# Kernel optimization log

Hardware: AMD Instinct MI355X
Metric: run time of the kernel (lower is better)

The kernel has to match this reference:

```python
import jax, jax.numpy as jnp
import numpy as np

NUM_HEADS = 8
NUM_HYPEREDGES = 64
NODE_DIM = 512
HEAD_DIM = NODE_DIM // NUM_HEADS
SCALING = float(np.sqrt(HEAD_DIM))


def setup_inputs() -> dict:
    key = jax.random.key(0)
    ks = jax.random.split(key, 6)
    B, N, D, M = 16, 4096, NODE_DIM, NUM_HYPEREDGES
    X = jax.random.normal(ks[0], (B, N, D), dtype=jnp.float32)
    # xavier_uniform for prototype_base [M, D]
    lim_p = float(np.sqrt(6.0 / (M + D)))
    prototype_base = jax.random.uniform(ks[1], (M, D), minval=-lim_p, maxval=lim_p, dtype=jnp.float32)
    # context_net: Linear(2D -> M*D), torch default init ~ U(-1/sqrt(fan_in), ...)
    lim_c = 1.0 / float(np.sqrt(2 * D))
    W_ctx = jax.random.uniform(ks[2], (M * D, 2 * D), minval=-lim_c, maxval=lim_c, dtype=jnp.float32)
    b_ctx = jax.random.uniform(ks[3], (M * D,), minval=-lim_c, maxval=lim_c, dtype=jnp.float32)
    # pre_head_proj: Linear(D -> D)
    lim_h = 1.0 / float(np.sqrt(D))
    W_pre = jax.random.uniform(ks[4], (D, D), minval=-lim_h, maxval=lim_h, dtype=jnp.float32)
    b_pre = jax.random.uniform(ks[5], (D,), minval=-lim_h, maxval=lim_h, dtype=jnp.float32)
    return {"X": X, "prototype_base": prototype_base, "W_ctx": W_ctx, "b_ctx": b_ctx,
            "W_pre": W_pre, "b_pre": b_pre}


def reference(X, prototype_base, W_ctx, b_ctx, W_pre, b_pre):
    B, N, D = X.shape
    M, H, hd = NUM_HYPEREDGES, NUM_HEADS, HEAD_DIM
    # context pooling: mean + max over nodes -> [B, 2D]
    ctx = jnp.concatenate([X.mean(axis=1), X.max(axis=1)], axis=-1)
    # per-batch prototype offsets: [B, M, D]
    offsets = (ctx @ W_ctx.T + b_ctx).reshape(B, M, D)
    prototypes = prototype_base[None, :, :] + offsets  # [B, M, D]
    # project nodes
    X_proj = X @ W_pre.T + b_pre  # [B, N, D]
    Xh = X_proj.reshape(B, N, H, hd)       # [B, N, H, hd]
    Ph = prototypes.reshape(B, M, H, hd)   # [B, M, H, hd]
    # per-head attention logits, mean over heads: [B, N, M]
    logits = jnp.einsum('bnhd,bmhd->bnm', Xh, Ph) / (SCALING * H)
    # dropout is identity in eval mode; softmax over the NODE axis (dim=1)
    return jax.nn.softmax(logits, axis=1)
```

## Files before the change

kernel.cpp:

```cpp
#include <hip/hip_runtime.h>
#include <math.h>

#define B_ 16
#define N_ 4096
#define D_ 512
#define M_ 64
#define MD 32768

typedef __attribute__((ext_vector_type(4))) float f32x4;
typedef __attribute__((ext_vector_type(8))) short short8;

#define OFF_PSUM   0
#define OFF_PMAXP  1048576
#define OFF_CTXB   2097152
#define OFF_PB     2105344
#define OFF_WPT    2367488
#define OFF_CB     2498560
#define OFF_GMAX   2499584
#define OFF_GINV   2500608
#define OFF_TPMAX  2501632
#define OFF_TPSUM  2763776
#define OFF_QB     3025920
#define OFF_LGB    3288064

__device__ __forceinline__ unsigned short f2bf(float f) {
    unsigned int u = __float_as_uint(f);
    u += 0x7fffu + ((u >> 16) & 1u);
    return (unsigned short)(u >> 16);
}
__device__ __forceinline__ float bf2f(unsigned short u) {
    return __uint_as_float(((unsigned int)u) << 16);
}

__global__ __launch_bounds__(256) void k_pool(const float* __restrict__ X, float* __restrict__ ws) {
    int b = blockIdx.x >> 6, nc = blockIdx.x & 63, t = threadIdx.x;
    int c = t & 127, p = t >> 7;
    const float4* X4 = (const float4*)X;
    float4 s = make_float4(0.f, 0.f, 0.f, 0.f);
    float4 mx = make_float4(-INFINITY, -INFINITY, -INFINITY, -INFINITY);
    int rowbase = b * N_ + nc * 64 + p;
#pragma unroll 8
    for (int i = 0; i < 32; i++) {
        int n = rowbase + 2 * i;
        float4 v = X4[n * 128 + c];
        s.x += v.x; s.y += v.y; s.z += v.z; s.w += v.w;
        mx.x = fmaxf(mx.x, v.x); mx.y = fmaxf(mx.y, v.y);
        mx.z = fmaxf(mx.z, v.z); mx.w = fmaxf(mx.w, v.w);
    }
    int slot = (b * 128 + nc * 2 + p) * 128 + c;
    ((float4*)(ws + OFF_PSUM))[slot] = s;
    ((float4*)(ws + OFF_PMAXP))[slot] = mx;
}

__global__ __launch_bounds__(256) void k_ctx(float* __restrict__ ws) {
    __shared__ f32x4 red[256];
    int b = blockIdx.x >> 2, q = blockIdx.x & 3, t = threadIdx.x;
    int lane = t & 63, w = t >> 6;
    bool isMax = (q >= 2);
    const f32x4* SRC = (const f32x4*)(ws + (isMax ? OFF_PMAXP : OFF_PSUM));
    int kk = (q & 1) * 64 + lane;
    f32x4 acc;
    if (isMax) acc = (f32x4){-INFINITY, -INFINITY, -INFINITY, -INFINITY};
    else       acc = (f32x4){0.f, 0.f, 0.f, 0.f};
#pragma unroll 8
    for (int i = 0; i < 32; i++) {
        int c = w * 32 + i;
        f32x4 v = SRC[(b * 128 + c) * 128 + kk];
        if (isMax) {
            acc[0] = fmaxf(acc[0], v[0]); acc[1] = fmaxf(acc[1], v[1]);
            acc[2] = fmaxf(acc[2], v[2]); acc[3] = fmaxf(acc[3], v[3]);
        } else {
            acc[0] += v[0]; acc[1] += v[1]; acc[2] += v[2]; acc[3] += v[3];
        }
    }
    red[t] = acc;
    __syncthreads();
    if (t < 64) {
        f32x4 a = red[t], b1 = red[64 + t], c1 = red[128 + t], d = red[192 + t];
        f32x4 r;
        if (isMax) {
#pragma unroll
            for (int j = 0; j < 4; j++) r[j] = fmaxf(fmaxf(a[j], b1[j]), fmaxf(c1[j], d[j]));
        } else {
#pragma unroll
            for (int j = 0; j < 4; j++) r[j] = (a[j] + b1[j] + c1[j] + d[j]) * (1.0f / 4096.0f);
        }
        ushort4 o;
        o.x = f2bf(r[0]); o.y = f2bf(r[1]); o.z = f2bf(r[2]); o.w = f2bf(r[3]);
        ((ushort4*)(ws + OFF_CTXB))[b * 256 + q * 64 + t] = o;
    }
}

__global__ __launch_bounds__(256) void k_protos(const float* __restrict__ Wc, const float* __restrict__ pb,
                                                const float* __restrict__ bc, float* __restrict__ ws) {
    int t = threadIdx.x;
    int wave = blockIdx.x * 4 + (t >> 6);
    int l = t & 63;
    int r0 = wave * 16;
    int row = r0 + (l & 15);
    int kg = l >> 4;
    const f32x4* W4 = (const f32x4*)Wc;
    const short8* CB8 = (const short8*)(ws + OFF_CTXB);
    f32x4 acc = (f32x4){0.f, 0.f, 0.f, 0.f};
    int wb = row * 256 + kg * 2;
    int cbase = (l & 15) * 128 + kg;
#pragma unroll 8
    for (int kc = 0; kc < 32; kc++) {
        f32x4 xa = __builtin_nontemporal_load(W4 + wb + kc * 8);
        f32x4 xb = __builtin_nontemporal_load(W4 + wb + kc * 8 + 1);
        short8 wf;
        wf[0] = (short)f2bf(xa[0]); wf[1] = (short)f2bf(xa[1]);
        wf[2] = (short)f2bf(xa[2]); wf[3] = (short)f2bf(xa[3]);
        wf[4] = (short)f2bf(xb[0]); wf[5] = (short)f2bf(xb[1]);
        wf[6] = (short)f2bf(xb[2]); wf[7] = (short)f2bf(xb[3]);
        short8 cf = CB8[cbase + kc * 4];
        acc = __builtin_amdgcn_mfma_f32_16x16x32_bf16(cf, wf, acc, 0, 0, 0);
    }
    int r = r0 + (l & 15);
    float add = pb[r] + bc[r];
    unsigned short* Pb = (unsigned short*)(ws + OFF_PB);
#pragma unroll
    for (int i = 0; i < 4; i++) {
        int bb = kg * 4 + i;
        Pb[bb * MD + r] = f2bf(acc[i] + add);
    }
}

__global__ __launch_bounds__(256) void k_misc(const float* __restrict__ Wp, const float* __restrict__ bpre,
                                              float* __restrict__ ws) {
    __shared__ unsigned short lt[64][65];
    int bx = blockIdx.x, t = threadIdx.x;
    if (bx < 64) {
        int ti = bx >> 3, tj = bx & 7;
        int sub = t >> 6, lane = t & 63;
#pragma unroll
        for (int i = 0; i < 16; i++) {
            int dl = i * 4 + sub;
            int jl = lane;
            lt[jl][dl] = f2bf(Wp[(ti * 64 + dl) * 512 + tj * 64 + jl]);
        }
        __syncthreads();
        unsigned short* WT = (unsigned short*)(ws + OFF_WPT);
#pragma unroll
        for (int i = 0; i < 16; i++) {
            int jl = i * 4 + sub;
            int dl = lane;
            WT[(tj * 64 + jl) * 512 + ti * 64 + dl] = lt[jl][dl];
        }
    } else {
        int w = (bx - 64) * 4 + (t >> 6);
        int l = t & 63;
        int b = w >> 6, m = w & 63;
        const short8* Pb8 = (const short8*)((const unsigned short*)(ws + OFF_PB) + b * MD + m * 512);
        short8 p = Pb8[l];
        const float4* bp4 = (const float4*)bpre;
        float4 q0 = bp4[l * 2], q1 = bp4[l * 2 + 1];
        float s = bf2f((unsigned short)p[0]) * q0.x + bf2f((unsigned short)p[1]) * q0.y
                + bf2f((unsigned short)p[2]) * q0.z + bf2f((unsigned short)p[3]) * q0.w
                + bf2f((unsigned short)p[4]) * q1.x + bf2f((unsigned short)p[5]) * q1.y
                + bf2f((unsigned short)p[6]) * q1.z + bf2f((unsigned short)p[7]) * q1.w;
#pragma unroll
        for (int off = 1; off < 64; off <<= 1) s += __shfl_xor(s, off);
        if (l == 0) ws[OFF_CB + w] = s * (1.0f / 64.0f);
    }
}

__global__ __launch_bounds__(256) void k_q(float* __restrict__ ws) {
    int t = threadIdx.x;
    int b = blockIdx.x >> 5, ctile = blockIdx.x & 31;
    int mt = t >> 6, l = t & 63;
    int col = l & 15, kg = l >> 4;
    const short8* WT8 = (const short8*)((const unsigned short*)(ws + OFF_WPT));
    const short8* Pb8 = (const short8*)((const unsigned short*)(ws + OFF_PB));
    f32x4 acc = (f32x4){0.f, 0.f, 0.f, 0.f};
    int abase = (ctile * 16 + col) * 64 + kg;
    int bbase = (b * 64 + mt * 16 + col) * 64 + kg;
#pragma unroll 4
    for (int kc = 0; kc < 16; kc++) {
        short8 af = WT8[abase + kc * 4];
        short8 bf = Pb8[bbase + kc * 4];
        acc = __builtin_amdgcn_mfma_f32_16x16x32_bf16(af, bf, acc, 0, 0, 0);
    }
    int m = mt * 16 + col;
    unsigned short* Qb = (unsigned short*)(ws + OFF_QB);
    union { unsigned short u[4]; uint2 v; } pk;
#pragma unroll
    for (int i = 0; i < 4; i++) pk.u[i] = f2bf(acc[i] * (1.0f / 64.0f));
    *(uint2*)(Qb + (b * 64 + m) * 512 + ctile * 16 + kg * 4) = pk.v;
}

__global__ __launch_bounds__(256) void k_logits(const float* __restrict__ X, float* __restrict__ ws) {
    int t = threadIdx.x;
    int W = blockIdx.x * 4 + (t >> 6);
    int b = W >> 8, nt = W & 255;
    int l = t & 63, col = l & 15, kg = l >> 4;
    int nA = nt * 16 + col;
    const float4* X4 = (const float4*)X;
    const short8* Qb8 = (const short8*)((const unsigned short*)(ws + OFF_QB));
    f32x4 acc[4];
#pragma unroll
    for (int mt = 0; mt < 4; mt++) acc[mt] = (f32x4){0.f, 0.f, 0.f, 0.f};

    int xbase4 = ((b * N_ + nA) * D_) >> 2;
    int qbase8 = b * 4096 + col * 64 + kg;
#pragma unroll 2
    for (int kc = 0; kc < 16; kc++) {
        float4 xa = X4[xbase4 + kc * 8 + kg * 2];
        float4 xb = X4[xbase4 + kc * 8 + kg * 2 + 1];
        short8 af;
        af[0] = (short)f2bf(xa.x); af[1] = (short)f2bf(xa.y);
        af[2] = (short)f2bf(xa.z); af[3] = (short)f2bf(xa.w);
        af[4] = (short)f2bf(xb.x); af[5] = (short)f2bf(xb.y);
        af[6] = (short)f2bf(xb.z); af[7] = (short)f2bf(xb.w);
#pragma unroll
        for (int mt = 0; mt < 4; mt++) {
            short8 bfr = Qb8[qbase8 + mt * 1024 + kc * 4];
            acc[mt] = __builtin_amdgcn_mfma_f32_16x16x32_bf16(af, bfr, acc[mt], 0, 0, 0);
        }
    }
    const float* cb = ws + OFF_CB + b * 64;
    unsigned short* LGB = (unsigned short*)(ws + OFF_LGB) + b * (N_ * 64) + nt * 16 * 64;
#pragma unroll
    for (int mt = 0; mt < 4; mt++) {
        int m = mt * 16 + col;
        float c = cb[m];
        float v0 = acc[mt][0] + c, v1 = acc[mt][1] + c;
        float v2 = acc[mt][2] + c, v3 = acc[mt][3] + c;
        int nr = kg * 4;
        LGB[(nr + 0) * 64 + m] = f2bf(v0);
        LGB[(nr + 1) * 64 + m] = f2bf(v1);
        LGB[(nr + 2) * 64 + m] = f2bf(v2);
        LGB[(nr + 3) * 64 + m] = f2bf(v3);
        float mx = fmaxf(fmaxf(v0, v1), fmaxf(v2, v3));
        mx = fmaxf(mx, __shfl_xor(mx, 16));
        mx = fmaxf(mx, __shfl_xor(mx, 32));
        float s = expf(v0 - mx) + expf(v1 - mx) + expf(v2 - mx) + expf(v3 - mx);
        s += __shfl_xor(s, 16);
        s += __shfl_xor(s, 32);
        if (kg == 0) {
            ws[OFF_TPMAX + (b * 64 + m) * 256 + nt] = mx;
            ws[OFF_TPSUM + (b * 64 + m) * 256 + nt] = s;
        }
    }
}

__global__ __launch_bounds__(256) void k_combine(float* __restrict__ ws) {
    int t = threadIdx.x;
    int w = blockIdx.x * 4 + (t >> 6);
    int l = t & 63;
    float4 a  = ((const float4*)(ws + OFF_TPMAX + w * 256))[l];
    float4 s4 = ((const float4*)(ws + OFF_TPSUM + w * 256))[l];
    float g = fmaxf(fmaxf(a.x, a.y), fmaxf(a.z, a.w));
    float s = s4.x * expf(a.x - g) + s4.y * expf(a.y - g)
            + s4.z * expf(a.z - g) + s4.w * expf(a.w - g);
#pragma unroll
    for (int off = 1; off < 64; off <<= 1) {
        float og = __shfl_xor(g, off);
        float os = __shfl_xor(s, off);
        float ng = fmaxf(g, og);
        s = s * expf(g - ng) + os * expf(og - ng);
        g = ng;
    }
    if (l == 0) { ws[OFF_GMAX + w] = g; ws[OFF_GINV + w] = 1.0f / s; }
}

__global__ __launch_bounds__(256) void k_final(const float* __restrict__ ws, float* __restrict__ out) {
    int idx = blockIdx.x * 256 + threadIdx.x;
    int flat = idx * 8;
    int b = flat >> 18;
    int m0 = flat & 63;
    uint4 lg = ((const uint4*)((const unsigned short*)(ws + OFF_LGB)))[idx];
    int bm = b * 64 + m0;
    float4 ga = *(const float4*)(ws + OFF_GMAX + bm);
    float4 gb = *(const float4*)(ws + OFF_GMAX + bm + 4);
    float4 ia = *(const float4*)(ws + OFF_GINV + bm);
    float4 ib = *(const float4*)(ws + OFF_GINV + bm + 4);
    float4 o0, o1;
    o0.x = expf(__uint_as_float(lg.x << 16)         - ga.x) * ia.x;
    o0.y = expf(__uint_as_float(lg.x & 0xffff0000u) - ga.y) * ia.y;
    o0.z = expf(__uint_as_float(lg.y << 16)         - ga.z) * ia.z;
    o0.w = expf(__uint_as_float(lg.y & 0xffff0000u) - ga.w) * ia.w;
    o1.x = expf(__uint_as_float(lg.z << 16)         - gb.x) * ib.x;
    o1.y = expf(__uint_as_float(lg.z & 0xffff0000u) - gb.y) * ib.y;
    o1.z = expf(__uint_as_float(lg.w << 16)         - gb.z) * ib.z;
    o1.w = expf(__uint_as_float(lg.w & 0xffff0000u) - gb.w) * ib.w;
    ((float4*)out)[idx * 2]     = o0;
    ((float4*)out)[idx * 2 + 1] = o1;
}

extern "C" void kernel_launch(void* const* d_in, const int* in_sizes, int n_in,
                              void* d_out, int out_size, void* d_ws, size_t ws_size,
                              hipStream_t stream) {
    const float* X  = (const float*)d_in[0];
    const float* pb = (const float*)d_in[1];
    const float* Wc = (const float*)d_in[2];
    const float* bc = (const float*)d_in[3];
    const float* Wp = (const float*)d_in[4];
    const float* bp = (const float*)d_in[5];
    float* ws  = (float*)d_ws;
    float* out = (float*)d_out;

    k_pool<<<1024, 256, 0, stream>>>(X, ws);
    k_ctx<<<64, 256, 0, stream>>>(ws);
    k_protos<<<512, 256, 0, stream>>>(Wc, pb, bc, ws);
    k_misc<<<320, 256, 0, stream>>>(Wp, bp, ws);
    k_q<<<512, 256, 0, stream>>>(ws);
    k_logits<<<1024, 256, 0, stream>>>(X, ws);
    k_combine<<<256, 256, 0, stream>>>(ws);
    k_final<<<2048, 256, 0, stream>>>(ws, out);
}
```

Measured before the change: 140.3 us.

## Fuse all phases into one cooperative kernel with grid-wide syncs

Replaces the eight separate kernel launches with a single cooperative persistent kernel of 512 blocks that runs each phase in turn, separated by grid.sync barriers. Phases that used more blocks loop over virtual block indices, and the small ctx and W_pre transpose phases now run concurrently in the same stage. The goal is to remove per-launch overhead and inter-kernel gaps. In exchange, occupancy is capped at 512 blocks (2 per CU under the launch bounds), the heavy pool and logits phases lose parallelism, and every stage now pays for a grid barrier.

```diff
diff --git a/kernel.cpp b/kernel.cpp
--- a/kernel.cpp
+++ b/kernel.cpp
@@ -1,5 +1,8 @@
 #include <hip/hip_runtime.h>
+#include <hip/hip_cooperative_groups.h>
 #include <math.h>
+
+namespace cg = cooperative_groups;
 
 #define B_ 16
 #define N_ 4096
@@ -32,8 +35,9 @@
     return __uint_as_float(((unsigned int)u) << 16);
 }
 
-__global__ __launch_bounds__(256) void k_pool(const float* __restrict__ X, float* __restrict__ ws) {
-    int b = blockIdx.x >> 6, nc = blockIdx.x & 63, t = threadIdx.x;
+
+__device__ __forceinline__ void ph_pool(int bid, int t, const float* X, float* ws) {
+    int b = bid >> 6, nc = bid & 63;
     int c = t & 127, p = t >> 7;
     const float4* X4 = (const float4*)X;
     float4 s = make_float4(0.f, 0.f, 0.f, 0.f);
@@ -52,9 +56,9 @@
     ((float4*)(ws + OFF_PMAXP))[slot] = mx;
 }
 
-__global__ __launch_bounds__(256) void k_ctx(float* __restrict__ ws) {
-    __shared__ f32x4 red[256];
-    int b = blockIdx.x >> 2, q = blockIdx.x & 3, t = threadIdx.x;
+__device__ __forceinline__ void ph_ctx(int bid, int t, float* ws, char* smem) {
+    f32x4* red = (f32x4*)smem;
+    int b = bid >> 2, q = bid & 3;
     int lane = t & 63, w = t >> 6;
     bool isMax = (q >= 2);
     const f32x4* SRC = (const f32x4*)(ws + (isMax ? OFF_PMAXP : OFF_PSUM));
@@ -89,12 +93,33 @@
         o.x = f2bf(r[0]); o.y = f2bf(r[1]); o.z = f2bf(r[2]); o.w = f2bf(r[3]);
         ((ushort4*)(ws + OFF_CTXB))[b * 256 + q * 64 + t] = o;
     }
-}
-
-__global__ __launch_bounds__(256) void k_protos(const float* __restrict__ Wc, const float* __restrict__ pb,
-                                                const float* __restrict__ bc, float* __restrict__ ws) {
-    int t = threadIdx.x;
-    int wave = blockIdx.x * 4 + (t >> 6);
+    __syncthreads();
+}
+
+__device__ __forceinline__ void ph_wpt(int bx, int t, const float* Wp, float* ws, char* smem) {
+    unsigned short (*lt)[65] = (unsigned short(*)[65])smem;
+    int ti = bx >> 3, tj = bx & 7;
+    int sub = t >> 6, lane = t & 63;
+#pragma unroll
+    for (int i = 0; i < 16; i++) {
+        int dl = i * 4 + sub;
+        int jl = lane;
+        lt[jl][dl] = f2bf(Wp[(ti * 64 + dl) * 512 + tj * 64 + jl]);
+    }
+    __syncthreads();
+    unsigned short* WT = (unsigned short*)(ws + OFF_WPT);
+#pragma unroll
+    for (int i = 0; i < 16; i++) {
+        int jl = i * 4 + sub;
+        int dl = lane;
+        WT[(tj * 64 + jl) * 512 + ti * 64 + dl] = lt[jl][dl];
+    }
+    __syncthreads();
+}
+
+__device__ __forceinline__ void ph_protos(int bid, int t, const float* Wc, const float* pb,
+                                          const float* bc, float* ws) {
+    int wave = bid * 4 + (t >> 6);
     int l = t & 63;
     int r0 = wave * 16;
     int row = r0 + (l & 15);
@@ -126,48 +151,8 @@
     }
 }
 
-__global__ __launch_bounds__(256) void k_misc(const float* __restrict__ Wp, const float* __restrict__ bpre,
-                                              float* __restrict__ ws) {
-    __shared__ unsigned short lt[64][65];
-    int bx = blockIdx.x, t = threadIdx.x;
-    if (bx < 64) {
-        int ti = bx >> 3, tj = bx & 7;
-        int sub = t >> 6, lane = t & 63;
-#pragma unroll
-        for (int i = 0; i < 16; i++) {
-            int dl = i * 4 + sub;
-            int jl = lane;
-            lt[jl][dl] = f2bf(Wp[(ti * 64 + dl) * 512 + tj * 64 + jl]);
-        }
-        __syncthreads();
-        unsigned short* WT = (unsigned short*)(ws + OFF_WPT);
-#pragma unroll
-        for (int i = 0; i < 16; i++) {
-            int jl = i * 4 + sub;
-            int dl = lane;
-            WT[(tj * 64 + jl) * 512 + ti * 64 + dl] = lt[jl][dl];
-        }
-    } else {
-        int w = (bx - 64) * 4 + (t >> 6);
-        int l = t & 63;
-        int b = w >> 6, m = w & 63;
-        const short8* Pb8 = (const short8*)((const unsigned short*)(ws + OFF_PB) + b * MD + m * 512);
-        short8 p = Pb8[l];
-        const float4* bp4 = (const float4*)bpre;
-        float4 q0 = bp4[l * 2], q1 = bp4[l * 2 + 1];
-        float s = bf2f((unsigned short)p[0]) * q0.x + bf2f((unsigned short)p[1]) * q0.y
-                + bf2f((unsigned short)p[2]) * q0.z + bf2f((unsigned short)p[3]) * q0.w
-                + bf2f((unsigned short)p[4]) * q1.x + bf2f((unsigned short)p[5]) * q1.y
-                + bf2f((unsigned short)p[6]) * q1.z + bf2f((unsigned short)p[7]) * q1.w;
-#pragma unroll
-        for (int off = 1; off < 64; off <<= 1) s += __shfl_xor(s, off);
-        if (l == 0) ws[OFF_CB + w] = s * (1.0f / 64.0f);
-    }
-}
-
-__global__ __launch_bounds__(256) void k_q(float* __restrict__ ws) {
-    int t = threadIdx.x;
-    int b = blockIdx.x >> 5, ctile = blockIdx.x & 31;
+__device__ __forceinline__ void ph_q(int bid, int t, float* ws) {
+    int b = bid >> 5, ctile = bid & 31;
     int mt = t >> 6, l = t & 63;
     int col = l & 15, kg = l >> 4;
     const short8* WT8 = (const short8*)((const unsigned short*)(ws + OFF_WPT));
@@ -189,9 +174,25 @@
     *(uint2*)(Qb + (b * 64 + m) * 512 + ctile * 16 + kg * 4) = pk.v;
 }
 
-__global__ __launch_bounds__(256) void k_logits(const float* __restrict__ X, float* __restrict__ ws) {
-    int t = threadIdx.x;
-    int W = blockIdx.x * 4 + (t >> 6);
+__device__ __forceinline__ void ph_cb(int w4, int t, const float* bpre, float* ws) {
+    int w = w4 * 4 + (t >> 6);
+    int l = t & 63;
+    int b = w >> 6, m = w & 63;
+    const short8* Pb8 = (const short8*)((const unsigned short*)(ws + OFF_PB) + b * MD + m * 512);
+    short8 p = Pb8[l];
+    const float4* bp4 = (const float4*)bpre;
+    float4 q0 = bp4[l * 2], q1 = bp4[l * 2 + 1];
+    float s = bf2f((unsigned short)p[0]) * q0.x + bf2f((unsigned short)p[1]) * q0.y
+            + bf2f((unsigned short)p[2]) * q0.z + bf2f((unsigned short)p[3]) * q0.w
+            + bf2f((unsigned short)p[4]) * q1.x + bf2f((unsigned short)p[5]) * q1.y
+            + bf2f((unsigned short)p[6]) * q1.z + bf2f((unsigned short)p[7]) * q1.w;
+#pragma unroll
+    for (int off = 1; off < 64; off <<= 1) s += __shfl_xor(s, off);
+    if (l == 0) ws[OFF_CB + w] = s * (1.0f / 64.0f);
+}
+
+__device__ __forceinline__ void ph_logits(int bid, int t, const float* X, float* ws) {
+    int W = bid * 4 + (t >> 6);
     int b = W >> 8, nt = W & 255;
     int l = t & 63, col = l & 15, kg = l >> 4;
     int nA = nt * 16 + col;
@@ -244,9 +245,8 @@
     }
 }
 
-__global__ __launch_bounds__(256) void k_combine(float* __restrict__ ws) {
-    int t = threadIdx.x;
-    int w = blockIdx.x * 4 + (t >> 6);
+__device__ __forceinline__ void ph_combine(int bid, int t, float* ws) {
+    int w = bid * 4 + (t >> 6);
     int l = t & 63;
     float4 a  = ((const float4*)(ws + OFF_TPMAX + w * 256))[l];
     float4 s4 = ((const float4*)(ws + OFF_TPSUM + w * 256))[l];
@@ -264,8 +264,8 @@
     if (l == 0) { ws[OFF_GMAX + w] = g; ws[OFF_GINV + w] = 1.0f / s; }
 }
 
-__global__ __launch_bounds__(256) void k_final(const float* __restrict__ ws, float* __restrict__ out) {
-    int idx = blockIdx.x * 256 + threadIdx.x;
+__device__ __forceinline__ void ph_final(int vb, int t, const float* ws, float* out) {
+    int idx = vb * 256 + t;
     int flat = idx * 8;
     int b = flat >> 18;
     int m0 = flat & 63;
@@ -288,6 +288,36 @@
     ((float4*)out)[idx * 2 + 1] = o1;
 }
 
+__global__ __launch_bounds__(256, 2) void k_mega(const float* X, const float* pb,
+                                                 const float* Wc, const float* bc,
+                                                 const float* Wp, const float* bp,
+                                                 float* ws, float* out) {
+    __shared__ __align__(16) char smem[8448];
+    cg::grid_group grid = cg::this_grid();
+    int bid = blockIdx.x, t = threadIdx.x;
+
+    ph_pool(bid, t, X, ws);
+    ph_pool(bid + 512, t, X, ws);
+    grid.sync();
+    if (bid < 64)        ph_ctx(bid, t, ws, smem);
+    else if (bid < 128)  ph_wpt(bid - 64, t, Wp, ws, smem);
+    grid.sync();
+    ph_protos(bid, t, Wc, pb, bc, ws);
+    grid.sync();
+    ph_q(bid, t, ws);
+    if (bid < 256) ph_cb(bid, t, bp, ws);
+    grid.sync();
+    ph_logits(bid, t, X, ws);
+    ph_logits(bid + 512, t, X, ws);
+    grid.sync();
+    if (bid < 256) ph_combine(bid, t, ws);
+    grid.sync();
+    ph_final(bid, t, ws, out);
+    ph_final(bid + 512, t, ws, out);
+    ph_final(bid + 1024, t, ws, out);
+    ph_final(bid + 1536, t, ws, out);
+}
+
 extern "C" void kernel_launch(void* const* d_in, const int* in_sizes, int n_in,
                               void* d_out, int out_size, void* d_ws, size_t ws_size,
                               hipStream_t stream) {
@@ -300,12 +330,7 @@
     float* ws  = (float*)d_ws;
     float* out = (float*)d_out;
 
-    k_pool<<<1024, 256, 0, stream>>>(X, ws);
-    k_ctx<<<64, 256, 0, stream>>>(ws);
-    k_protos<<<512, 256, 0, stream>>>(Wc, pb, bc, ws);
-    k_misc<<<320, 256, 0, stream>>>(Wp, bp, ws);
-    k_q<<<512, 256, 0, stream>>>(ws);
-    k_logits<<<1024, 256, 0, stream>>>(X, ws);
-    k_combine<<<256, 256, 0, stream>>>(ws);
-    k_final<<<2048, 256, 0, stream>>>(ws, out);
-}
+    void* kargs[] = {(void*)&X, (void*)&pb, (void*)&Wc, (void*)&bc,
+                     (void*)&Wp, (void*)&bp, (void*)&ws, (void*)&out};
+    hipLaunchCooperativeKernel((void*)k_mega, dim3(512), dim3(256), kargs, 0, stream);
+}
```

Result: slower. 508.6 us (+262.6%).
